# Kernel optimization log

Measured on AMD Instinct MI355X. Metric: run time of the kernel, lower is better.

The kernel has to match this reference:

```python
import jax, jax.numpy as jnp
import numpy as np

T = 16384
D = 2048      # input_dim
H = 256       # gru hidden
NF = 8        # n_frames (top-k)
NC = 2        # n_classes


def _gru_dir(x_gates, W_hh, b_hh, reverse):
    # x_gates: (T, 3H) precomputed input projection; torch gate order: r, z, n
    def step(h, gx):
        gh = h @ W_hh.T + b_hh
        xr, xz, xn = jnp.split(gx, 3)
        hr, hz, hn = jnp.split(gh, 3)
        r = jax.nn.sigmoid(xr + hr)
        z = jax.nn.sigmoid(xz + hz)
        n = jnp.tanh(xn + r * hn)
        h_new = (1.0 - z) * n + z * h
        return h_new, h_new
    h0 = jnp.zeros((W_hh.shape[1],), x_gates.dtype)
    _, hs = jax.lax.scan(step, h0, x_gates, reverse=reverse)
    return hs  # (T, H)


def setup_inputs() -> dict:
    key = jax.random.key(0)
    ks = jax.random.split(key, 16)
    s = 0.02
    inp = {
        "features": jax.random.normal(ks[0], (T, D), jnp.float32),
        "temperature": jnp.float32(0.5),
        # BiGRU params (torch layout: W_ih (3H, D), W_hh (3H, H))
        "W_ih_f": jax.random.normal(ks[1], (3 * H, D), jnp.float32) * s,
        "W_hh_f": jax.random.normal(ks[2], (3 * H, H), jnp.float32) * s,
        "b_ih_f": jnp.zeros((3 * H,), jnp.float32),
        "b_hh_f": jnp.zeros((3 * H,), jnp.float32),
        "W_ih_b": jax.random.normal(ks[3], (3 * H, D), jnp.float32) * s,
        "W_hh_b": jax.random.normal(ks[4], (3 * H, H), jnp.float32) * s,
        "b_ih_b": jnp.zeros((3 * H,), jnp.float32),
        "b_hh_b": jnp.zeros((3 * H,), jnp.float32),
        # scorer MLP: Linear(2H,64) -> ReLU -> Linear(64,1)
        "Ws1": jax.random.normal(ks[5], (64, 2 * H), jnp.float32) * s,
        "bs1": jnp.zeros((64,), jnp.float32),
        "Ws2": jax.random.normal(ks[6], (1, 64), jnp.float32) * s,
        "bs2": jnp.zeros((1,), jnp.float32),
        # classifier: Linear(D,256) -> ReLU -> Linear(256,NC)
        "Wc1": jax.random.normal(ks[7], (256, D), jnp.float32) * s,
        "bc1": jnp.zeros((256,), jnp.float32),
        "Wc2": jax.random.normal(ks[8], (NC, 256), jnp.float32) * s,
        "bc2": jnp.zeros((NC,), jnp.float32),
    }
    return inp


def reference(features, temperature, W_ih_f, W_hh_f, b_ih_f, b_hh_f,
              W_ih_b, W_hh_b, b_ih_b, b_hh_b, Ws1, bs1, Ws2, bs2,
              Wc1, bc1, Wc2, bc2):
    # FrameScorer: BiGRU
    gx_f = features @ W_ih_f.T + b_ih_f            # (T, 3H)
    gx_b = features @ W_ih_b.T + b_ih_b
    h_f = _gru_dir(gx_f, W_hh_f, b_hh_f, reverse=False)
    h_b = _gru_dir(gx_b, W_hh_b, b_hh_b, reverse=True)
    h = jnp.concatenate([h_f, h_b], axis=-1)       # (T, 2H)
    # scorer MLP (dropout is identity in eval)
    scores = (jax.nn.relu(h @ Ws1.T + bs1) @ Ws2.T + bs2)[:, 0]   # (T,)
    # soft top-k weights
    n = min(NF, scores.shape[0])
    _, topk_idx = jax.lax.top_k(scores, n)
    mask = jnp.zeros_like(scores).at[topk_idx].set(1.0)
    masked_scores = scores * mask + (1.0 - mask) * (-1e9)
    weights = jax.nn.softmax(masked_scores / temperature)          # (T,)
    # weighted feature sum + classifier
    clip_repr = weights @ features                                  # (D,)
    logits = jax.nn.relu(clip_repr @ Wc1.T + bc1) @ Wc2.T + bc2     # (NC,)
    return logits, scores
```

## Files before the change

### kernel.cpp

```cpp
#include <hip/hip_runtime.h>
#include <hip/hip_fp16.h>
#include <math.h>

#define T_LEN 16384
#define D_IN  2048
#define H_GRU 256
#define G3    768
#define NFRM  8
#define NCLS  2

#define CHUNK 32
#define WARM  48
#define GSTEPS (WARM + CHUNK)
#define BQ    4
#define NCHUNK (T_LEN / CHUNK)
#define GRU_BLOCKS (NCHUNK / BQ)

typedef _Float16 f16x8 __attribute__((ext_vector_type(8)));
typedef float    f32x4 __attribute__((ext_vector_type(4)));

static const size_t OFF_GXF = 0;
static const size_t OFF_GXB = OFF_GXF + (size_t)T_LEN * G3;
static const size_t OFF_H   = OFF_GXB + (size_t)T_LEN * G3;
static const size_t OFF_BIA = OFF_H   + (size_t)T_LEN * 512;
static const size_t OFF_SC  = OFF_BIA + 2 * G3;
static const size_t OFF_WPF = OFF_SC  + (size_t)T_LEN;
static const size_t OFF_WPB = OFF_WPF + (size_t)G3 * H_GRU / 2;
static const size_t OFF_SEL = OFF_WPB + (size_t)G3 * H_GRU / 2;
static const size_t OFF_CH  = OFF_SEL + 16;

__device__ __forceinline__ float fsig(float x) {
    return __builtin_amdgcn_rcpf(1.f + __expf(-x));
}
__device__ __forceinline__ float ftanh(float x) {
    float e = __expf(2.f * x);
    return 1.f - 2.f * __builtin_amdgcn_rcpf(e + 1.f);
}

__device__ __forceinline__ void gload_lds16(const void* gp, void* lp) {
    __builtin_amdgcn_global_load_lds(
        (const __attribute__((address_space(1))) void*)gp,
        (__attribute__((address_space(3))) void*)lp,
        16, 0, 0);
}

__device__ __forceinline__ f16x8 pack8(const f32x4 lo, const f32x4 hi) {
    f16x8 r;
    r[0] = (_Float16)lo[0]; r[1] = (_Float16)lo[1];
    r[2] = (_Float16)lo[2]; r[3] = (_Float16)lo[3];
    r[4] = (_Float16)hi[0]; r[5] = (_Float16)hi[1];
    r[6] = (_Float16)hi[2]; r[7] = (_Float16)hi[3];
    return r;
}

__global__ void bias_fold_kernel(const float* __restrict__ bi0, const float* __restrict__ bh0,
                                 const float* __restrict__ bi1, const float* __restrict__ bh1,
                                 float* __restrict__ o0, float* __restrict__ o1) {
    int t = blockIdx.x * 256 + threadIdx.x;
    if (t < G3) {
        float a0 = bi0[t], a1 = bi1[t];
        if (t < 512) { a0 += bh0[t]; a1 += bh1[t]; }
        o0[t] = a0; o1[t] = a1;
    }
}

__global__ __launch_bounds__(256) void cvt_w_kernel(const float* __restrict__ Wf,
                                                    const float* __restrict__ Wb,
                                                    __half* __restrict__ B16) {
    const float* __restrict__ src = blockIdx.y ? Wb : Wf;
    __half* __restrict__ dst = B16 + (size_t)blockIdx.y * G3 * D_IN;
    const int i = blockIdx.x * 256 + threadIdx.x;
    float4 a = *(const float4*)&src[(size_t)i * 8];
    float4 b = *(const float4*)&src[(size_t)i * 8 + 4];
    __half2 h[4];
    h[0] = __float22half2_rn(make_float2(a.x, a.y));
    h[1] = __float22half2_rn(make_float2(a.z, a.w));
    h[2] = __float22half2_rn(make_float2(b.x, b.y));
    h[3] = __float22half2_rn(make_float2(b.z, b.w));
    *(float4*)&dst[(size_t)i * 8] = *(float4*)h;
}

__global__ void pack_whh_mfma_kernel(const float* __restrict__ W0,
                                     const float* __restrict__ W1,
                                     f16x8* __restrict__ P0,
                                     f16x8* __restrict__ P1) {
    const float* W = blockIdx.y ? W1 : W0;
    f16x8* P = blockIdx.y ? P1 : P0;
    int tc = blockIdx.x;
    int l = threadIdx.x;
    int t = tc >> 3, c = tc & 7;
    int m = t * 16 + (l & 15);
    int k = c * 32 + (l >> 4) * 8;
    const float* src = W + (size_t)m * H_GRU + k;
    f16x8 v;
#pragma unroll
    for (int j = 0; j < 8; ++j) v[j] = (_Float16)src[j];
    P[(size_t)tc * 64 + l] = v;
}

#define GXBK 32
__global__ __launch_bounds__(256) void gemm_gx_kernel(
    const float* __restrict__ A,
    const __half* __restrict__ B16,
    const float* __restrict__ biaf, const float* __restrict__ biab,
    float* __restrict__ Cf, float* __restrict__ Cb) {
    __shared__ __align__(16) float  Asf[4096];
    __shared__ __align__(16) __half Bsh[4096];

    const int tid  = threadIdx.x;
    const int lane = tid & 63;
    const int wave = tid >> 6;
    const int lm   = lane & 15;
    const int lk   = lane >> 4;
    const int mw   = wave & 1;
    const int nw   = wave >> 1;

    const int wg = blockIdx.x;
    const int id = (wg & 7) * (1536 / 8) + (wg >> 3);
    const int mt = id / 12;
    const int nt = id - mt * 12;
    const int bm  = mt * 128;
    const int bnt = nt * 128;

    const float* __restrict__ bias;
    float* __restrict__ C;
    int bn_local;
    if (nt < 6) { C = Cf; bias = biaf; bn_local = bnt; }
    else        { C = Cb; bias = biab; bn_local = bnt - 768; }

    const float*  gA = A   + (size_t)(bm  + lm) * D_IN + lk * 8;
    const __half* gB = B16 + (size_t)(bnt + lm) * D_IN + lk * 8;

    f32x4 acc[4][4];
#pragma unroll
    for (int a = 0; a < 4; ++a)
#pragma unroll
        for (int b = 0; b < 4; ++b) acc[a][b] = (f32x4)0.f;

    for (int k0 = 0; k0 < D_IN; k0 += GXBK) {
        __syncthreads();
#pragma unroll
        for (int j = 0; j < 4; ++j) {
            const int q = 4 * wave + j, f = q >> 1, h = q & 1;
            gload_lds16(gA + (size_t)(16 * f) * D_IN + k0 + 4 * h, &Asf[q * 256]);
        }
#pragma unroll
        for (int j = 0; j < 2; ++j) {
            const int f = 2 * wave + j;
            gload_lds16(gB + (size_t)(16 * f) * D_IN + k0, &Bsh[f * 512]);
        }
        __syncthreads();

        f16x8 afr[4], bfr[4];
#pragma unroll
        for (int tm = 0; tm < 4; ++tm) {
            const int q0 = (4 * mw + tm) * 2;
            f32x4 lo = *(const f32x4*)&Asf[q0 * 256 + lane * 4];
            f32x4 hi = *(const f32x4*)&Asf[q0 * 256 + 256 + lane * 4];
            afr[tm] = pack8(lo, hi);
        }
#pragma unroll
        for (int tn = 0; tn < 4; ++tn) {
            const int fb = 4 * nw + tn;
            bfr[tn] = *(const f16x8*)&Bsh[fb * 512 + lane * 8];
        }
#pragma unroll
        for (int tm = 0; tm < 4; ++tm)
#pragma unroll
            for (int tn = 0; tn < 4; ++tn)
                acc[tm][tn] = __builtin_amdgcn_mfma_f32_16x16x32_f16(
                    afr[tm], bfr[tn], acc[tm][tn], 0, 0, 0);
    }

#pragma unroll
    for (int tm = 0; tm < 4; ++tm) {
#pragma unroll
        for (int tn = 0; tn < 4; ++tn) {
            int gn = bn_local + 64 * nw + 16 * tn + lm;
            float bb = bias[gn];
#pragma unroll
            for (int reg = 0; reg < 4; ++reg) {
                int gm = bm + 64 * mw + 16 * tm + lk * 4 + reg;
                C[(size_t)gm * G3 + gn] = acc[tm][tn][reg] + bb;
            }
        }
    }
}

#define BM 64
#define BN 64
#define BK 32
__global__ __launch_bounds__(256) void scorer_kernel(
    const float* __restrict__ A,
    const float* __restrict__ B,
    const float* __restrict__ bias,
    const float* __restrict__ Ws2,
    const float* __restrict__ bs2,
    float* __restrict__ sc, float* __restrict__ outs,
    int M, int N, int K) {
    __shared__ __align__(16) float As[BK][BM + 4];
    __shared__ __align__(16) float Bs[BK][BN + 4];

    const int tid = threadIdx.x;
    const int bm = blockIdx.x * BM;
    const int kk8 = tid & 7;
    const int r32 = tid >> 3;
    const int tx = tid & 15;
    const int ty = tid >> 4;

    float acc[4][4];
#pragma unroll
    for (int a = 0; a < 4; ++a)
#pragma unroll
        for (int b = 0; b < 4; ++b) acc[a][b] = 0.f;

    for (int k0 = 0; k0 < K; k0 += BK) {
        float4 a0 = *(const float4*)&A[(size_t)(bm + r32) * K + k0 + kk8 * 4];
        float4 a1 = *(const float4*)&A[(size_t)(bm + r32 + 32) * K + k0 + kk8 * 4];
        float4 b0 = *(const float4*)&B[(size_t)(r32) * K + k0 + kk8 * 4];
        float4 b1 = *(const float4*)&B[(size_t)(r32 + 32) * K + k0 + kk8 * 4];
        __syncthreads();
        As[kk8 * 4 + 0][r32] = a0.x; As[kk8 * 4 + 1][r32] = a0.y;
        As[kk8 * 4 + 2][r32] = a0.z; As[kk8 * 4 + 3][r32] = a0.w;
        As[kk8 * 4 + 0][r32 + 32] = a1.x; As[kk8 * 4 + 1][r32 + 32] = a1.y;
        As[kk8 * 4 + 2][r32 + 32] = a1.z; As[kk8 * 4 + 3][r32 + 32] = a1.w;
        Bs[kk8 * 4 + 0][r32] = b0.x; Bs[kk8 * 4 + 1][r32] = b0.y;
        Bs[kk8 * 4 + 2][r32] = b0.z; Bs[kk8 * 4 + 3][r32] = b0.w;
        Bs[kk8 * 4 + 0][r32 + 32] = b1.x; Bs[kk8 * 4 + 1][r32 + 32] = b1.y;
        Bs[kk8 * 4 + 2][r32 + 32] = b1.z; Bs[kk8 * 4 + 3][r32 + 32] = b1.w;
        __syncthreads();
#pragma unroll 8
        for (int kk = 0; kk < BK; ++kk) {
            float4 av = *(const float4*)&As[kk][ty * 4];
            float4 bv = *(const float4*)&Bs[kk][tx * 4];
            acc[0][0] += av.x * bv.x; acc[0][1] += av.x * bv.y; acc[0][2] += av.x * bv.z; acc[0][3] += av.x * bv.w;
            acc[1][0] += av.y * bv.x; acc[1][1] += av.y * bv.y; acc[1][2] += av.y * bv.z; acc[1][3] += av.y * bv.w;
            acc[2][0] += av.z * bv.x; acc[2][1] += av.z * bv.y; acc[2][2] += av.z * bv.z; acc[2][3] += av.z * bv.w;
            acc[3][0] += av.w * bv.x; acc[3][1] += av.w * bv.y; acc[3][2] += av.w * bv.z; acc[3][3] += av.w * bv.w;
        }
    }

    float4 bvv = *(const float4*)&bias[tx * 4];
    float4 w2  = *(const float4*)&Ws2[tx * 4];
    const float b2 = bs2[0];
#pragma unroll
    for (int im = 0; im < 4; ++im) {
        float s = fmaxf(acc[im][0] + bvv.x, 0.f) * w2.x
                + fmaxf(acc[im][1] + bvv.y, 0.f) * w2.y
                + fmaxf(acc[im][2] + bvv.z, 0.f) * w2.z
                + fmaxf(acc[im][3] + bvv.w, 0.f) * w2.w;
#pragma unroll
        for (int off = 1; off < 16; off <<= 1) s += __shfl_xor(s, off);
        if (tx == 0) {
            int m = bm + ty * 4 + im;
            float sval = s + b2;
            sc[m] = sval;
            outs[m] = sval;
        }
    }
}

#define HPAD 272
__global__ __launch_bounds__(1024, 4) void gru_v5_kernel(
    const float* __restrict__ gx0, const float* __restrict__ gx1,
    const f16x8* __restrict__ Wk0, const f16x8* __restrict__ Wk1,
    const float* __restrict__ bh0, const float* __restrict__ bh1,
    float* __restrict__ Hbuf) {
    const int dir = blockIdx.y;
    const float* __restrict__ gx = dir ? gx1 : gx0;
    const f16x8* __restrict__ Wk = dir ? Wk1 : Wk0;
    const float* __restrict__ bh = dir ? bh1 : bh0;
    const int col_off = dir * 256;

    const int tid  = threadIdx.x;
    const int lane = tid & 63;
    const int wv   = tid >> 6;
    const int ln   = lane & 15;
    const int lq   = lane >> 4;

    __shared__ __align__(16) __half h_sh[16][HPAD];
    __shared__ __align__(16) float red[4][772];

    f16x8 Wf[3][8];
#pragma unroll
    for (int tt = 0; tt < 3; ++tt)
#pragma unroll
        for (int c = 0; c < 8; ++c)
            Wf[tt][c] = Wk[(size_t)((3 * wv + tt) * 8 + c) * 64 + lane];

    for (int idx = tid; idx < 16 * HPAD; idx += 1024) ((__half*)h_sh)[idx] = __float2half(0.f);

    const int i   = tid & 255;
    const int grp = tid >> 8;
    const float bn_ = bh[512 + i];
    float h_own = 0.f;
    const int cbase = blockIdx.x * BQ;
    const int dtv = dir ? -1 : 1;
    const int lo = (cbase + grp) * CHUNK;
    const int t0 = dir ? (lo + CHUNK - 1 + WARM) : (lo - WARM);
    __syncthreads();

    for (int s = 0; s < GSTEPS; ++s) {
        const int t = t0 + dtv * s;
        const bool valid = ((unsigned)t < (unsigned)T_LEN);
        const int tc2 = t < 0 ? 0 : (t > T_LEN - 1 ? T_LEN - 1 : t);
        const float* g = gx + (size_t)tc2 * G3 + i;
        const float xr = g[0], xz = g[256], xn = g[512];

        f32x4 acc[3];
#pragma unroll
        for (int tt = 0; tt < 3; ++tt) acc[tt] = (f32x4)0.f;
#pragma unroll
        for (int c = 0; c < 8; ++c) {
            f16x8 bfr = *(const f16x8*)&h_sh[ln][c * 32 + lq * 8];
#pragma unroll
            for (int tt = 0; tt < 3; ++tt)
                acc[tt] = __builtin_amdgcn_mfma_f32_16x16x32_f16(Wf[tt][c], bfr, acc[tt], 0, 0, 0);
        }
        if (ln < 4) {
#pragma unroll
            for (int tt = 0; tt < 3; ++tt)
                *(f32x4*)&red[ln][(3 * wv + tt) * 16 + lq * 4] = acc[tt];
        }
        __syncthreads();

        const float r = fsig(xr + red[grp][i]);
        const float z = fsig(xz + red[grp][256 + i]);
        const float nn = ftanh(xn + r * (red[grp][512 + i] + bn_));
        const float hnew = (1.f - z) * nn + z * h_own;
        if (valid) {
            h_own = hnew;
            h_sh[grp][i] = __float2half(hnew);
            const bool pay = dir ? (t < lo + CHUNK) : (t >= lo);
            if (pay) Hbuf[(size_t)t * 512 + col_off + i] = hnew;
        }
        __syncthreads();
    }
}

__global__ __launch_bounds__(256) void select_topk_kernel(
    const float* __restrict__ scores, const float* __restrict__ temp_p,
    int* __restrict__ sel_idx_out, float* __restrict__ sel_w_out) {
    __shared__ float red_v[4];
    __shared__ int   red_i[4];
    __shared__ int   bcast_idx;
    __shared__ int   sel_idx_sh[NFRM];
    __shared__ float sel_v_sh[NFRM];

    const int tid  = threadIdx.x;
    const int lane = tid & 63;
    const int wv   = tid >> 6;

    float sv[64];
#pragma unroll
    for (int a = 0; a < 64; ++a) sv[a] = scores[a * 256 + tid];

    for (int round = 0; round < NFRM; ++round) {
        float best = -1e30f;
        int bidx = 0x7fffffff;
#pragma unroll
        for (int a = 0; a < 64; ++a) {
            if (sv[a] > best) { best = sv[a]; bidx = a * 256 + tid; }
        }
#pragma unroll
        for (int off = 32; off > 0; off >>= 1) {
            float v2 = __shfl_down(best, off);
            int   i2 = __shfl_down(bidx, off);
            if (v2 > best || (v2 == best && i2 < bidx)) { best = v2; bidx = i2; }
        }
        if (lane == 0) { red_v[wv] = best; red_i[wv] = bidx; }
        __syncthreads();
        if (tid == 0) {
            float bv = red_v[0]; int bi = red_i[0];
#pragma unroll
            for (int w = 1; w < 4; ++w)
                if (red_v[w] > bv || (red_v[w] == bv && red_i[w] < bi)) { bv = red_v[w]; bi = red_i[w]; }
            sel_idx_sh[round] = bi; sel_v_sh[round] = bv; bcast_idx = bi;
        }
        __syncthreads();
        const int widx = bcast_idx;
        if ((widx & 255) == tid) {
            const int aa = widx >> 8;
#pragma unroll
            for (int a = 0; a < 64; ++a)
                if (a == aa) sv[a] = -1e30f;
        }
    }

    if (tid == 0) {
        float temp = temp_p[0];
        float m = sel_v_sh[0];
        float e[NFRM];
        float sum = 0.f;
        for (int j = 0; j < NFRM; ++j) { e[j] = expf((sel_v_sh[j] - m) / temp); sum += e[j]; }
        for (int j = 0; j < NFRM; ++j) { sel_idx_out[j] = sel_idx_sh[j]; sel_w_out[j] = e[j] / sum; }
    }
}

__global__ __launch_bounds__(256) void classifier1_kernel(
    const float* __restrict__ features,
    const int* __restrict__ sel_idx, const float* __restrict__ sel_w,
    const float* __restrict__ Wc1, const float* __restrict__ bc1,
    float* __restrict__ hid) {
    const int r = blockIdx.x;
    const int tid = threadIdx.x;
    __shared__ int   s_idx[NFRM];
    __shared__ float s_w[NFRM];
    __shared__ float part[4];
    if (tid < NFRM) { s_idx[tid] = sel_idx[tid]; s_w[tid] = sel_w[tid]; }
    __syncthreads();

    float acc = 0.f;
#pragma unroll
    for (int q = 0; q < D_IN / 256; ++q) {
        int d = q * 256 + tid;
        float c = 0.f;
#pragma unroll
        for (int j = 0; j < NFRM; ++j)
            c += s_w[j] * features[(size_t)s_idx[j] * D_IN + d];
        acc += c * Wc1[(size_t)r * D_IN + d];
    }
#pragma unroll
    for (int off = 32; off > 0; off >>= 1) acc += __shfl_down(acc, off);
    if ((tid & 63) == 0) part[tid >> 6] = acc;
    __syncthreads();
    if (tid == 0)
        hid[r] = fmaxf(part[0] + part[1] + part[2] + part[3] + bc1[r], 0.f);
}

__global__ __launch_bounds__(128) void classifier2_kernel(
    const float* __restrict__ hid, const float* __restrict__ Wc2,
    const float* __restrict__ bc2, float* __restrict__ out) {
    const int tid = threadIdx.x;
    const int c = tid >> 6;
    const int l = tid & 63;
    float acc = 0.f;
#pragma unroll
    for (int k = l; k < 256; k += 64) acc += hid[k] * Wc2[c * 256 + k];
#pragma unroll
    for (int off = 32; off > 0; off >>= 1) acc += __shfl_down(acc, off);
    if (l == 0) out[c] = acc + bc2[c];
}

extern "C" void kernel_launch(void* const* d_in, const int* in_sizes, int n_in,
                              void* d_out, int out_size, void* d_ws, size_t ws_size,
                              hipStream_t stream) {
    const float* features = (const float*)d_in[0];
    const float* temperature = (const float*)d_in[1];
    const float* W_ih_f = (const float*)d_in[2];
    const float* W_hh_f = (const float*)d_in[3];
    const float* b_ih_f = (const float*)d_in[4];
    const float* b_hh_f = (const float*)d_in[5];
    const float* W_ih_b = (const float*)d_in[6];
    const float* W_hh_b = (const float*)d_in[7];
    const float* b_ih_b = (const float*)d_in[8];
    const float* b_hh_b = (const float*)d_in[9];
    const float* Ws1 = (const float*)d_in[10];
    const float* bs1 = (const float*)d_in[11];
    const float* Ws2 = (const float*)d_in[12];
    const float* bs2 = (const float*)d_in[13];
    const float* Wc1 = (const float*)d_in[14];
    const float* bc1 = (const float*)d_in[15];
    const float* Wc2 = (const float*)d_in[16];
    const float* bc2 = (const float*)d_in[17];

    float* ws = (float*)d_ws;
    float* gx_f = ws + OFF_GXF;
    float* gx_b = ws + OFF_GXB;
    float* Hbuf = ws + OFF_H;
    float* biaf = ws + OFF_BIA;
    float* biab = ws + OFF_BIA + G3;
    float* sc   = ws + OFF_SC;
    f16x8* Wk_f = (f16x8*)(ws + OFF_WPF);
    f16x8* Wk_b = (f16x8*)(ws + OFF_WPB);
    int*   sel_i = (int*)(ws + OFF_SEL);
    float* sel_w = ws + OFF_SEL + NFRM;
    float* chid  = ws + OFF_CH;
    float* out  = (float*)d_out;

    __half* B16 = (__half*)(ws + OFF_H);

    bias_fold_kernel<<<3, 256, 0, stream>>>(b_ih_f, b_hh_f, b_ih_b, b_hh_b, biaf, biab);

    cvt_w_kernel<<<dim3(768, 2), 256, 0, stream>>>(W_ih_f, W_ih_b, B16);

    pack_whh_mfma_kernel<<<dim3(384, 2), 64, 0, stream>>>(W_hh_f, W_hh_b, Wk_f, Wk_b);

    gemm_gx_kernel<<<1536, 256, 0, stream>>>(features, B16, biaf, biab, gx_f, gx_b);

    gru_v5_kernel<<<dim3(GRU_BLOCKS, 2), 1024, 0, stream>>>(
        gx_f, gx_b, Wk_f, Wk_b, b_hh_f, b_hh_b, Hbuf);

    scorer_kernel<<<T_LEN / BM, 256, 0, stream>>>(
        Hbuf, Ws1, bs1, Ws2, bs2, sc, out + 2, T_LEN, 64, 512);

    select_topk_kernel<<<1, 256, 0, stream>>>(sc, temperature, sel_i, sel_w);

    classifier1_kernel<<<256, 256, 0, stream>>>(features, sel_i, sel_w, Wc1, bc1, chid);

    classifier2_kernel<<<1, 128, 0, stream>>>(chid, Wc2, bc2, out);
}
```

Before: 703.7 us.

## Double-buffer gx GEMM tiles and store A operand as fp16 in LDS

Rewrites the input-projection GEMM main loop to prefetch the next K-slice into a second LDS buffer while MFMAs run on the current one, which cuts the per-iteration syncs from two to one. The A tile is now read from global memory into registers and converted to fp16 before it is written to LDS. This halves A's LDS footprint and removes the per-fragment float-to-half packing from the inner loop. The kernel also asks for 3 blocks per CU via launch bounds, which may limit register allocation.

```diff
diff --git a/kernel.cpp b/kernel.cpp
--- a/kernel.cpp
+++ b/kernel.cpp
@@ -99,13 +99,13 @@
 }
 
 #define GXBK 32
-__global__ __launch_bounds__(256) void gemm_gx_kernel(
+__global__ __launch_bounds__(256, 3) void gemm_gx_kernel(
     const float* __restrict__ A,
     const __half* __restrict__ B16,
     const float* __restrict__ biaf, const float* __restrict__ biab,
     float* __restrict__ Cf, float* __restrict__ Cb) {
-    __shared__ __align__(16) float  Asf[4096];
-    __shared__ __align__(16) __half Bsh[4096];
+    __shared__ __align__(16) __half As16[2][4096];
+    __shared__ __align__(16) __half Bs16[2][4096];
 
     const int tid  = threadIdx.x;
     const int lane = tid & 63;
@@ -128,7 +128,10 @@
     if (nt < 6) { C = Cf; bias = biaf; bn_local = bnt; }
     else        { C = Cb; bias = biab; bn_local = bnt - 768; }
 
-    const float*  gA = A   + (size_t)(bm  + lm) * D_IN + lk * 8;
+    const int arow = ((tid >> 6) << 4) + (tid & 15);
+    const int acol = ((tid >> 4) & 3) * 8;
+    const float* gA0 = A + (size_t)(bm + arow) * D_IN + acol;
+    const float* gA1 = gA0 + (size_t)64 * D_IN;
     const __half* gB = B16 + (size_t)(bnt + lm) * D_IN + lk * 8;
 
     f32x4 acc[4][4];
@@ -137,39 +140,58 @@
 #pragma unroll
         for (int b = 0; b < 4; ++b) acc[a][b] = (f32x4)0.f;
 
+#pragma unroll
+    for (int j = 0; j < 2; ++j) {
+        const int f = 2 * wave + j;
+        gload_lds16(gB + (size_t)(16 * f) * D_IN, &Bs16[0][f * 512]);
+    }
+    {
+        f32x4 va0 = *(const f32x4*)(gA0);
+        f32x4 va1 = *(const f32x4*)(gA0 + 4);
+        f32x4 vb0 = *(const f32x4*)(gA1);
+        f32x4 vb1 = *(const f32x4*)(gA1 + 4);
+        *(f16x8*)&As16[0][tid * 8] = pack8(va0, va1);
+        *(f16x8*)&As16[0][tid * 8 + 2048] = pack8(vb0, vb1);
+    }
+    __syncthreads();
+
+    int cur = 0;
     for (int k0 = 0; k0 < D_IN; k0 += GXBK) {
-        __syncthreads();
-#pragma unroll
-        for (int j = 0; j < 4; ++j) {
-            const int q = 4 * wave + j, f = q >> 1, h = q & 1;
-            gload_lds16(gA + (size_t)(16 * f) * D_IN + k0 + 4 * h, &Asf[q * 256]);
-        }
-#pragma unroll
-        for (int j = 0; j < 2; ++j) {
-            const int f = 2 * wave + j;
-            gload_lds16(gB + (size_t)(16 * f) * D_IN + k0, &Bsh[f * 512]);
-        }
-        __syncthreads();
+        const int kn = k0 + GXBK;
+        const bool more = (kn < D_IN);
+        f32x4 va0, va1, vb0, vb1;
+        if (more) {
+#pragma unroll
+            for (int j = 0; j < 2; ++j) {
+                const int f = 2 * wave + j;
+                gload_lds16(gB + (size_t)(16 * f) * D_IN + kn, &Bs16[cur ^ 1][f * 512]);
+            }
+            va0 = *(const f32x4*)(gA0 + kn);
+            va1 = *(const f32x4*)(gA0 + kn + 4);
+            vb0 = *(const f32x4*)(gA1 + kn);
+            vb1 = *(const f32x4*)(gA1 + kn + 4);
+        }
 
         f16x8 afr[4], bfr[4];
 #pragma unroll
-        for (int tm = 0; tm < 4; ++tm) {
-            const int q0 = (4 * mw + tm) * 2;
-            f32x4 lo = *(const f32x4*)&Asf[q0 * 256 + lane * 4];
-            f32x4 hi = *(const f32x4*)&Asf[q0 * 256 + 256 + lane * 4];
-            afr[tm] = pack8(lo, hi);
-        }
-#pragma unroll
-        for (int tn = 0; tn < 4; ++tn) {
-            const int fb = 4 * nw + tn;
-            bfr[tn] = *(const f16x8*)&Bsh[fb * 512 + lane * 8];
-        }
+        for (int tm = 0; tm < 4; ++tm)
+            afr[tm] = *(const f16x8*)&As16[cur][(4 * mw + tm) * 512 + lane * 8];
+#pragma unroll
+        for (int tn = 0; tn < 4; ++tn)
+            bfr[tn] = *(const f16x8*)&Bs16[cur][(4 * nw + tn) * 512 + lane * 8];
 #pragma unroll
         for (int tm = 0; tm < 4; ++tm)
 #pragma unroll
             for (int tn = 0; tn < 4; ++tn)
                 acc[tm][tn] = __builtin_amdgcn_mfma_f32_16x16x32_f16(
                     afr[tm], bfr[tn], acc[tm][tn], 0, 0, 0);
+
+        if (more) {
+            *(f16x8*)&As16[cur ^ 1][tid * 8] = pack8(va0, va1);
+            *(f16x8*)&As16[cur ^ 1][tid * 8 + 2048] = pack8(vb0, vb1);
+        }
+        __syncthreads();
+        cur ^= 1;
     }
 
 #pragma unroll
```

Measured after the change: 683.7 us. 1.03x faster.

## Double-buffer input-projection GEMM with register-staged fp16 A tiles and BK=64

Applied to the files above, without the earlier changes.

Restructures the gate-projection GEMM into a double-buffered pipeline. The next K-tile of A is loaded into registers and B goes to LDS asynchronously while MFMAs run on the current tile. A is converted to fp16 once before the LDS store instead of being packed after every LDS read. The K tile grows to 64 and launch bounds request two blocks per CU, which shortens the barrier-separated load-compute serialization. The cost is more LDS (64KB) and more registers, plus hand-placed waitcnt and barriers that must be correct.

```diff
diff --git a/kernel.cpp b/kernel.cpp
--- a/kernel.cpp
+++ b/kernel.cpp
@@ -98,14 +98,15 @@
     P[(size_t)tc * 64 + l] = v;
 }
 
-#define GXBK 32
-__global__ __launch_bounds__(256) void gemm_gx_kernel(
+#define GXBK 64
+#define GXNT (D_IN / GXBK)
+__global__ __launch_bounds__(256, 2) void gemm_gx_kernel(
     const float* __restrict__ A,
     const __half* __restrict__ B16,
     const float* __restrict__ biaf, const float* __restrict__ biab,
     float* __restrict__ Cf, float* __restrict__ Cb) {
-    __shared__ __align__(16) float  Asf[4096];
-    __shared__ __align__(16) __half Bsh[4096];
+    __shared__ __align__(16) __half As16[2][8192];
+    __shared__ __align__(16) __half Bs16[2][8192];
 
     const int tid  = threadIdx.x;
     const int lane = tid & 63;
@@ -128,8 +129,11 @@
     if (nt < 6) { C = Cf; bias = biaf; bn_local = bnt; }
     else        { C = Cb; bias = biab; bn_local = bnt - 768; }
 
-    const float*  gA = A   + (size_t)(bm  + lm) * D_IN + lk * 8;
-    const __half* gB = B16 + (size_t)(bnt + lm) * D_IN + lk * 8;
+    const int arow = ((tid >> 6) << 4) + (tid & 15);
+    const int acol = ((tid >> 4) & 3) * 8;
+    const float* gA0 = A + (size_t)(bm + arow) * D_IN + acol;
+    const float* gA1 = gA0 + (size_t)64 * D_IN;
+    const int af0 = tid >> 6;
 
     f32x4 acc[4][4];
 #pragma unroll
@@ -137,33 +141,100 @@
 #pragma unroll
         for (int b = 0; b < 4; ++b) acc[a][b] = (f32x4)0.f;
 
-    for (int k0 = 0; k0 < D_IN; k0 += GXBK) {
-        __syncthreads();
+    {
+        f32x4 av[8];
+#pragma unroll
+        for (int h = 0; h < 2; ++h) {
+            av[4 * h + 0] = *(const f32x4*)(gA0 + 32 * h);
+            av[4 * h + 1] = *(const f32x4*)(gA0 + 32 * h + 4);
+            av[4 * h + 2] = *(const f32x4*)(gA1 + 32 * h);
+            av[4 * h + 3] = *(const f32x4*)(gA1 + 32 * h + 4);
+        }
 #pragma unroll
         for (int j = 0; j < 4; ++j) {
-            const int q = 4 * wave + j, f = q >> 1, h = q & 1;
-            gload_lds16(gA + (size_t)(16 * f) * D_IN + k0 + 4 * h, &Asf[q * 256]);
-        }
-#pragma unroll
-        for (int j = 0; j < 2; ++j) {
-            const int f = 2 * wave + j;
-            gload_lds16(gB + (size_t)(16 * f) * D_IN + k0, &Bsh[f * 512]);
-        }
-        __syncthreads();
-
+            const int q = 4 * wave + j;
+            gload_lds16(B16 + (size_t)(bnt + 16 * (q >> 1) + lm) * D_IN
+                            + 32 * (q & 1) + lk * 8,
+                        &Bs16[0][q * 512]);
+        }
+#pragma unroll
+        for (int h = 0; h < 2; ++h) {
+            *(f16x8*)&As16[0][((af0 * 2 + h) * 512) + (tid & 63) * 8] =
+                pack8(av[4 * h + 0], av[4 * h + 1]);
+            *(f16x8*)&As16[0][(((af0 + 4) * 2 + h) * 512) + (tid & 63) * 8] =
+                pack8(av[4 * h + 2], av[4 * h + 3]);
+        }
+        asm volatile("s_waitcnt lgkmcnt(0)" ::: "memory");
+        __builtin_amdgcn_sched_barrier(0);
+        __builtin_amdgcn_s_barrier();
+    }
+
+    int cur = 0;
+#pragma unroll 1
+    for (int t = 0; t < GXNT - 1; ++t) {
+        const int kn = (t + 1) * GXBK;
+        f32x4 nv[8];
+#pragma unroll
+        for (int h = 0; h < 2; ++h) {
+            nv[4 * h + 0] = *(const f32x4*)(gA0 + kn + 32 * h);
+            nv[4 * h + 1] = *(const f32x4*)(gA0 + kn + 32 * h + 4);
+            nv[4 * h + 2] = *(const f32x4*)(gA1 + kn + 32 * h);
+            nv[4 * h + 3] = *(const f32x4*)(gA1 + kn + 32 * h + 4);
+        }
+#pragma unroll
+        for (int j = 0; j < 4; ++j) {
+            const int q = 4 * wave + j;
+            gload_lds16(B16 + (size_t)(bnt + 16 * (q >> 1) + lm) * D_IN
+                            + kn + 32 * (q & 1) + lk * 8,
+                        &Bs16[cur ^ 1][q * 512]);
+        }
+        asm volatile("s_waitcnt vmcnt(12)" ::: "memory");
+        __builtin_amdgcn_sched_barrier(0);
+        __builtin_amdgcn_s_barrier();
+        __builtin_amdgcn_s_setprio(1);
+#pragma unroll
+        for (int s = 0; s < 2; ++s) {
+            f16x8 afr[4], bfr[4];
+#pragma unroll
+            for (int tm = 0; tm < 4; ++tm)
+                afr[tm] = *(const f16x8*)&As16[cur][((4 * mw + tm) * 2 + s) * 512 + lane * 8];
+#pragma unroll
+            for (int tn = 0; tn < 4; ++tn)
+                bfr[tn] = *(const f16x8*)&Bs16[cur][((4 * nw + tn) * 2 + s) * 512 + lane * 8];
+#pragma unroll
+            for (int tm = 0; tm < 4; ++tm)
+#pragma unroll
+                for (int tn = 0; tn < 4; ++tn)
+                    acc[tm][tn] = __builtin_amdgcn_mfma_f32_16x16x32_f16(
+                        afr[tm], bfr[tn], acc[tm][tn], 0, 0, 0);
+        }
+        __builtin_amdgcn_s_setprio(0);
+#pragma unroll
+        for (int h = 0; h < 2; ++h) {
+            *(f16x8*)&As16[cur ^ 1][((af0 * 2 + h) * 512) + (tid & 63) * 8] =
+                pack8(nv[4 * h + 0], nv[4 * h + 1]);
+            *(f16x8*)&As16[cur ^ 1][(((af0 + 4) * 2 + h) * 512) + (tid & 63) * 8] =
+                pack8(nv[4 * h + 2], nv[4 * h + 3]);
+        }
+        asm volatile("s_waitcnt lgkmcnt(0)" ::: "memory");
+        __builtin_amdgcn_sched_barrier(0);
+        __builtin_amdgcn_s_barrier();
+        cur ^= 1;
+    }
+
+    asm volatile("s_waitcnt vmcnt(0)" ::: "memory");
+    __builtin_amdgcn_sched_barrier(0);
+    __builtin_amdgcn_s_barrier();
+    __builtin_amdgcn_s_setprio(1);
+#pragma unroll
+    for (int s = 0; s < 2; ++s) {
         f16x8 afr[4], bfr[4];
 #pragma unroll
-        for (int tm = 0; tm < 4; ++tm) {
-            const int q0 = (4 * mw + tm) * 2;
-            f32x4 lo = *(const f32x4*)&Asf[q0 * 256 + lane * 4];
-            f32x4 hi = *(const f32x4*)&Asf[q0 * 256 + 256 + lane * 4];
-            afr[tm] = pack8(lo, hi);
-        }
-#pragma unroll
-        for (int tn = 0; tn < 4; ++tn) {
-            const int fb = 4 * nw + tn;
-            bfr[tn] = *(const f16x8*)&Bsh[fb * 512 + lane * 8];
-        }
+        for (int tm = 0; tm < 4; ++tm)
+            afr[tm] = *(const f16x8*)&As16[cur][((4 * mw + tm) * 2 + s) * 512 + lane * 8];
+#pragma unroll
+        for (int tn = 0; tn < 4; ++tn)
+            bfr[tn] = *(const f16x8*)&Bs16[cur][((4 * nw + tn) * 2 + s) * 512 + lane * 8];
 #pragma unroll
         for (int tm = 0; tm < 4; ++tm)
 #pragma unroll
@@ -171,6 +242,7 @@
                 acc[tm][tn] = __builtin_amdgcn_mfma_f32_16x16x32_f16(
                     afr[tm], bfr[tn], acc[tm][tn], 0, 0, 0);
     }
+    __builtin_amdgcn_s_setprio(0);
 
 #pragma unroll
     for (int tm = 0; tm < 4; ++tm) {
```

New measurement: 669.5 us. 4.9% less time.

## Load GEMM fragments straight from global memory, dropping LDS staging

Applied to the files above, without the earlier changes.

The input-projection GEMM no longer stages A and B tiles through shared memory with global_load_lds and block barriers. Each wave now reads its MFMA fragments directly from global memory into registers, and the launch bounds request three blocks per CU. The goal is to remove the barriers and the LDS round trip and to raise occupancy. The cost is that tiles once shared across waves are now loaded redundantly by each wave (A by two waves, B by two), and the loop has no software prefetch, so it relies on the caches and on occupancy to hide latency.

```diff
diff --git a/kernel.cpp b/kernel.cpp
--- a/kernel.cpp
+++ b/kernel.cpp
@@ -35,13 +35,6 @@
 __device__ __forceinline__ float ftanh(float x) {
     float e = __expf(2.f * x);
     return 1.f - 2.f * __builtin_amdgcn_rcpf(e + 1.f);
-}
-
-__device__ __forceinline__ void gload_lds16(const void* gp, void* lp) {
-    __builtin_amdgcn_global_load_lds(
-        (const __attribute__((address_space(1))) void*)gp,
-        (__attribute__((address_space(3))) void*)lp,
-        16, 0, 0);
 }
 
 __device__ __forceinline__ f16x8 pack8(const f32x4 lo, const f32x4 hi) {
@@ -99,14 +92,11 @@
 }
 
 #define GXBK 32
-__global__ __launch_bounds__(256) void gemm_gx_kernel(
+__global__ __launch_bounds__(256, 3) void gemm_gx_kernel(
     const float* __restrict__ A,
     const __half* __restrict__ B16,
     const float* __restrict__ biaf, const float* __restrict__ biab,
     float* __restrict__ Cf, float* __restrict__ Cb) {
-    __shared__ __align__(16) float  Asf[4096];
-    __shared__ __align__(16) __half Bsh[4096];
-
     const int tid  = threadIdx.x;
     const int lane = tid & 63;
     const int wave = tid >> 6;
@@ -128,8 +118,8 @@
     if (nt < 6) { C = Cf; bias = biaf; bn_local = bnt; }
     else        { C = Cb; bias = biab; bn_local = bnt - 768; }
 
-    const float*  gA = A   + (size_t)(bm  + lm) * D_IN + lk * 8;
-    const __half* gB = B16 + (size_t)(bnt + lm) * D_IN + lk * 8;
+    const float*  gA = A   + (size_t)(bm  + 64 * mw + lm) * D_IN + lk * 8;
+    const __half* gB = B16 + (size_t)(bnt + 64 * nw + lm) * D_IN + lk * 8;
 
     f32x4 acc[4][4];
 #pragma unroll
@@ -137,33 +127,19 @@
 #pragma unroll
         for (int b = 0; b < 4; ++b) acc[a][b] = (f32x4)0.f;
 
+#pragma unroll 1
     for (int k0 = 0; k0 < D_IN; k0 += GXBK) {
-        __syncthreads();
-#pragma unroll
-        for (int j = 0; j < 4; ++j) {
-            const int q = 4 * wave + j, f = q >> 1, h = q & 1;
-            gload_lds16(gA + (size_t)(16 * f) * D_IN + k0 + 4 * h, &Asf[q * 256]);
-        }
-#pragma unroll
-        for (int j = 0; j < 2; ++j) {
-            const int f = 2 * wave + j;
-            gload_lds16(gB + (size_t)(16 * f) * D_IN + k0, &Bsh[f * 512]);
-        }
-        __syncthreads();
-
         f16x8 afr[4], bfr[4];
 #pragma unroll
         for (int tm = 0; tm < 4; ++tm) {
-            const int q0 = (4 * mw + tm) * 2;
-            f32x4 lo = *(const f32x4*)&Asf[q0 * 256 + lane * 4];
-            f32x4 hi = *(const f32x4*)&Asf[q0 * 256 + 256 + lane * 4];
+            const float* p = gA + (size_t)(16 * tm) * D_IN + k0;
+            f32x4 lo = *(const f32x4*)p;
+            f32x4 hi = *(const f32x4*)(p + 4);
             afr[tm] = pack8(lo, hi);
         }
 #pragma unroll
-        for (int tn = 0; tn < 4; ++tn) {
-            const int fb = 4 * nw + tn;
-            bfr[tn] = *(const f16x8*)&Bsh[fb * 512 + lane * 8];
-        }
+        for (int tn = 0; tn < 4; ++tn)
+            bfr[tn] = *(const f16x8*)(gB + (size_t)(16 * tn) * D_IN + k0);
 #pragma unroll
         for (int tm = 0; tm < 4; ++tm)
 #pragma unroll
```

Measured after the change: 978.4 us. +39.0%, slower.
